# Kernel optimization log

Measured on AMD Instinct MI355X. Metric: run time of the kernel, lower is better.

The kernel has to match this reference:

```python
import jax, jax.numpy as jnp
import numpy as np
from jax import lax

C = 256          # channels
G = 16           # groups
Cg = C // G      # group channels
K = 3            # kernel size
P = K * K        # sampling points per group
PAD = 1          # spatial padding (dilation=1, stride=1)


def setup_inputs() -> dict:
    key = jax.random.key(0)
    ks = jax.random.split(key, 8)
    def rn(k, shape, s):
        return jax.random.normal(k, shape, dtype=jnp.float32) * s
    N, H, W = 4, 64, 64
    return {
        "x": jax.random.normal(ks[0], (N, C, H, W), dtype=jnp.float32),
        "w_in": rn(ks[1], (C, C), 0.02),
        "b_in": jnp.zeros((C,), jnp.float32),
        "dw_w": rn(ks[2], (C, 1, K, K), 0.1),   # depthwise conv, OIHW with I=1
        "dw_b": jnp.zeros((C,), jnp.float32),
        "ln_g": jnp.ones((C,), jnp.float32),
        "ln_b": jnp.zeros((C,), jnp.float32),
        "w_off": rn(ks[3], (C, G * P * 2), 0.01),
        "b_off": jnp.zeros((G * P * 2,), jnp.float32),
        "w_mask": rn(ks[4], (C, G * P), 0.01),
        "b_mask": jnp.zeros((G * P,), jnp.float32),
        "w_out": rn(ks[5], (C, C), 0.02),
        "b_out": jnp.zeros((C,), jnp.float32),
    }


def _layernorm(x, g, b, eps=1e-5):
    mu = jnp.mean(x, -1, keepdims=True)
    var = jnp.var(x, -1, keepdims=True)
    return (x - mu) * lax.rsqrt(var + eps) * g + b


def _dcnv3_core(xq, offset, mask, offset_scale=1.0):
    # xq: (N, Ho, Wo, C) channels-last value features (matches dcnv3_core_pytorch)
    N, Ho, Wo, _ = xq.shape
    xpad = jnp.pad(xq, ((0, 0), (PAD, PAD), (PAD, PAD), (0, 0)))
    Hi, Wi = Ho + 2 * PAD, Wo + 2 * PAD
    # reference points: pixel centers in padded coords, normalized by (Wi, Hi)
    ry = (jnp.arange(Ho, dtype=jnp.float32) + 0.5 + (K - 1) // 2) / Hi  # (Ho,)
    rx = (jnp.arange(Wo, dtype=jnp.float32) + 0.5 + (K - 1) // 2) / Wi  # (Wo,)
    # dilation grid, kw-major order as in _generate_dilation_grids
    kk = jnp.arange(K, dtype=jnp.float32) - (K - 1) // 2
    gx, gy = jnp.meshgrid(kk, kk, indexing='ij')   # gx over w, gy over h
    gpx = gx.reshape(-1) / Wi                      # (P,)
    gpy = gy.reshape(-1) / Hi
    off = offset.reshape(N, Ho, Wo, G, P, 2)
    # normalized sampling locations, shape (N, Ho, Wo, G, P)
    locx = rx[None, None, :, None, None] + gpx * offset_scale + off[..., 0] * (offset_scale / Wi)
    locy = ry[None, :, None, None, None] + gpy * offset_scale + off[..., 1] * (offset_scale / Hi)
    # grid_sample align_corners=False pixel coords
    px = locx * Wi - 0.5
    py = locy * Hi - 0.5
    x0f = jnp.floor(px); y0f = jnp.floor(py)
    fx = px - x0f; fy = py - y0f
    x0 = x0f.astype(jnp.int32); y0 = y0f.astype(jnp.int32)

    flat = jnp.transpose(xpad.reshape(N, Hi * Wi, G, Cg), (0, 2, 1, 3))  # (N,G,HiWi,Cg)

    def t(a):  # (N,Ho,Wo,G,P) -> (N,G,Ho*Wo,P)
        return jnp.transpose(a.reshape(N, Ho * Wo, G, P), (0, 2, 1, 3))

    def gather(ix, iy):
        valid = (ix >= 0) & (ix < Wi) & (iy >= 0) & (iy < Hi)
        idx = jnp.clip(iy, 0, Hi - 1) * Wi + jnp.clip(ix, 0, Wi - 1)
        idx_t = t(idx).reshape(N, G, Ho * Wo * P, 1)
        v = jnp.take_along_axis(flat, idx_t, axis=2).reshape(N, G, Ho * Wo, P, Cg)
        return v, t(valid).astype(xq.dtype)

    wx1, wy1 = t(fx), t(fy)
    wx0, wy0 = 1.0 - wx1, 1.0 - wy1
    v00, m00 = gather(x0, y0)
    v01, m01 = gather(x0 + 1, y0)
    v10, m10 = gather(x0, y0 + 1)
    v11, m11 = gather(x0 + 1, y0 + 1)
    samp = (v00 * (wx0 * wy0 * m00)[..., None] + v01 * (wx1 * wy0 * m01)[..., None]
            + v10 * (wx0 * wy1 * m10)[..., None] + v11 * (wx1 * wy1 * m11)[..., None])
    mk = t(mask)                                       # (N,G,HoWo,P)
    out = jnp.sum(samp * mk[..., None], axis=3)        # (N,G,HoWo,Cg)
    return jnp.transpose(out, (0, 2, 1, 3)).reshape(N, Ho, Wo, G * Cg)


def reference(x, w_in, b_in, dw_w, dw_b, ln_g, ln_b, w_off, b_off, w_mask, b_mask, w_out, b_out):
    N, _, H, W = x.shape
    x_nhwc = jnp.transpose(x, (0, 2, 3, 1))
    xq = x_nhwc @ w_in + b_in                          # input_proj (value branch)
    # offset/mask branch: depthwise 3x3 conv (channels_first) + LN + GELU
    x1 = lax.conv_general_dilated(x, dw_w, (1, 1), [(PAD, PAD), (PAD, PAD)],
                                  feature_group_count=C,
                                  dimension_numbers=('NCHW', 'OIHW', 'NCHW'))
    x1 = x1 + dw_b[None, :, None, None]
    x1 = jnp.transpose(x1, (0, 2, 3, 1))
    x1 = jax.nn.gelu(_layernorm(x1, ln_g, ln_b), approximate=False)
    offset = x1 @ w_off + b_off                        # (N,H,W,G*P*2)
    mask = x1 @ w_mask + b_mask                        # (N,H,W,G*P)
    mask = jax.nn.softmax(mask.reshape(N, H, W, G, P), axis=-1).reshape(N, H, W, G * P)
    y = _dcnv3_core(xq, offset, mask)
    y = y @ w_out + b_out                              # output_proj
    return jnp.transpose(y, (0, 3, 1, 2))              # back to channels_first
```

## Files before the change

### kernel.cpp

```cpp
#include <hip/hip_runtime.h>
#include <math.h>

#define CCH 256
#define HP2 68
#define WP2 68

typedef __attribute__((ext_vector_type(8))) short bf16x8;
typedef __attribute__((ext_vector_type(8))) unsigned short u16x8;
typedef __attribute__((ext_vector_type(4))) float f32x4;

__device__ __forceinline__ unsigned short f2bf(float f) {
    unsigned int u = __float_as_uint(f);
    unsigned int r = (u + 0x7fffu + ((u >> 16) & 1u)) >> 16;
    return (unsigned short)r;
}
__device__ __forceinline__ float bf2f(unsigned short h) {
    return __uint_as_float(((unsigned int)h) << 16);
}

#define OFF_XNBF   0ull
#define OFF_XPAD   8388608ull
#define OFF_X1BF   17858560ull
#define OFF_OFFS   26247168ull
#define OFF_MASK   35684352ull
#define OFF_WTIN   40402944ull
#define OFF_WTOFF  40534016ull
#define OFF_WTMSK  40681472ull
#define OFF_WTOUT  40755200ull
#define OFF_BOM    40886272ull
#define OFF_DWT    40888064ull

__global__ __launch_bounds__(256) void prep(const float* __restrict__ x,
                                            unsigned short* __restrict__ xo,
                                            unsigned int* __restrict__ xpadz,
                                            const float* __restrict__ w_in,
                                            const float* __restrict__ w_off,
                                            const float* __restrict__ w_mask,
                                            const float* __restrict__ w_out,
                                            unsigned short* __restrict__ wtin,
                                            unsigned short* __restrict__ wtoff,
                                            unsigned short* __restrict__ wtmsk,
                                            unsigned short* __restrict__ wtout,
                                            const float* __restrict__ b_off,
                                            const float* __restrict__ b_mask,
                                            float* __restrict__ bias_om,
                                            const float* __restrict__ dw_w,
                                            unsigned short* __restrict__ dwtb) {
    int z = blockIdx.z;
    int tx = threadIdx.x, ty = threadIdx.y;
    int t = ty * 32 + tx;
    if (z < 4) {
        int flat = (z * 8 + blockIdx.y) * 128 + blockIdx.x;
        for (unsigned int i = flat * 256 + t; i < 2367488u; i += 4096u * 256u) xpadz[i] = 0u;
        __shared__ float tt[32][33];
        int hw0 = blockIdx.x * 32, c0 = blockIdx.y * 32, n = z;
#pragma unroll
        for (int i = 0; i < 4; i++)
            tt[ty + i * 8][tx] = x[(size_t)(n * CCH + c0 + ty + i * 8) * 4096 + hw0 + tx];
        __syncthreads();
#pragma unroll
        for (int i = 0; i < 4; i++)
            xo[(size_t)(n * 4096 + hw0 + ty + i * 8) * CCH + c0 + tx] = f2bf(tt[tx][ty + i * 8]);
        return;
    }
    if (z == 8) {
        if (blockIdx.y == 0) {
            if (blockIdx.x < 2) {
                int i = blockIdx.x * 256 + t;
                if (i < 432) bias_om[i] = (i < 288) ? b_off[i] : b_mask[i - 288];
            } else if (blockIdx.x < 11) {
                int tap = blockIdx.x - 2;
                dwtb[tap * 256 + t] = f2bf(dw_w[t * 9 + tap]);
            }
        }
        return;
    }
    const float* w; unsigned short* wt; int N;
    if (z == 4)      { w = w_in;   wt = wtin;  N = 256; }
    else if (z == 5) { w = w_off;  wt = wtoff; N = 288; }
    else if (z == 6) { w = w_mask; wt = wtmsk; N = 144; }
    else             { w = w_out;  wt = wtout; N = 256; }
    const int K = 256;
    int n0 = blockIdx.x * 32, k0 = blockIdx.y * 32;
    if (n0 >= N) return;
    __shared__ float tb[32][33];
#pragma unroll
    for (int i = 0; i < 4; i++) {
        int k = k0 + ty + i * 8;
        if (n0 + tx < N) tb[ty + i * 8][tx] = w[(size_t)k * N + n0 + tx];
    }
    __syncthreads();
#pragma unroll
    for (int i = 0; i < 4; i++) {
        int n = n0 + ty + i * 8;
        if (n < N) wt[(size_t)n * K + k0 + tx] = f2bf(tb[tx][ty + i * 8]);
    }
}

template<int MODE>
__device__ __forceinline__ void gemm_tile(const unsigned short* __restrict__ A,
                                          const unsigned short* __restrict__ Bt,
                                          const float* __restrict__ bias,
                                          void* __restrict__ C0, void* __restrict__ C1,
                                          int N, int K, int bm, int bn, int tid) {
    int wid = tid >> 6, lane = tid & 63;
    int wr = wid >> 1, wc = wid & 1;
    int row0 = bm + wr * 64, col0 = bn + wc * 64;
    int lr = lane & 15, kg = lane >> 4;
    f32x4 acc[4][4];
#pragma unroll
    for (int i = 0; i < 4; i++)
#pragma unroll
        for (int j = 0; j < 4; j++) acc[i][j] = (f32x4){0.f, 0.f, 0.f, 0.f};

    const unsigned short* Ap = A + (size_t)(row0 + lr) * K + kg * 8;
    const unsigned short* Bp[4];
    bool bok[4];
#pragma unroll
    for (int j = 0; j < 4; j++) {
        int c = col0 + j * 16 + lr;
        bok[j] = (c < N);
        Bp[j] = Bt + (size_t)(bok[j] ? c : 0) * K + kg * 8;
    }
    const bf16x8 bzero = {0, 0, 0, 0, 0, 0, 0, 0};
    for (int k0 = 0; k0 < K; k0 += 32) {
        bf16x8 a[4], b[4];
#pragma unroll
        for (int i = 0; i < 4; i++)
            a[i] = *(const bf16x8*)(Ap + (size_t)i * 16 * K + k0);
#pragma unroll
        for (int j = 0; j < 4; j++)
            b[j] = bok[j] ? *(const bf16x8*)(Bp[j] + k0) : bzero;
        __builtin_amdgcn_s_setprio(1);
#pragma unroll
        for (int i = 0; i < 4; i++)
#pragma unroll
            for (int j = 0; j < 4; j++)
                acc[i][j] = __builtin_amdgcn_mfma_f32_16x16x32_bf16(a[i], b[j], acc[i][j], 0, 0, 0);
        __builtin_amdgcn_s_setprio(0);
    }
#pragma unroll
    for (int i = 0; i < 4; i++) {
#pragma unroll
        for (int j = 0; j < 4; j++) {
            int col = col0 + j * 16 + lr;
            if (col >= N) continue;
            float bc = (MODE == 4) ? 0.f : bias[col];
#pragma unroll
            for (int r = 0; r < 4; r++) {
                int m = row0 + i * 16 + kg * 4 + r;
                float val = acc[i][j][r] + bc;
                if (MODE == 1) {
                    int n = m >> 12, hw = m & 4095, h = hw >> 6, w = hw & 63;
                    ((unsigned short*)C0)[(size_t)((n * HP2 + h + 2) * WP2 + (w + 2)) * CCH + col] = f2bf(val);
                } else if (MODE == 4) {
                    int n = col >> 12, hw = col & 4095;
                    ((float*)C0)[(size_t)(n * CCH + m) * 4096 + hw] = val + bias[m];
                } else {
                    if (col < 288)
                        ((unsigned short*)C0)[(size_t)m * 288 + col] = f2bf(val);
                    else
                        ((unsigned short*)C1)[(size_t)m * 144 + (col - 288)] = f2bf(val);
                }
            }
        }
    }
}

template<int MODE>
__global__ __launch_bounds__(256) void gemm_mfma(const unsigned short* __restrict__ A,
                                                 const unsigned short* __restrict__ Bt,
                                                 const float* __restrict__ bias,
                                                 void* __restrict__ C0,
                                                 void* __restrict__ C1,
                                                 int N, int K) {
    gemm_tile<MODE>(A, Bt, bias, C0, C1, N, K, blockIdx.y * 128, blockIdx.x * 128, threadIdx.x);
}

__global__ __launch_bounds__(256) void stage2(const unsigned short* __restrict__ xnbf,
                                              const unsigned short* __restrict__ wtin,
                                              const float* __restrict__ b_in,
                                              unsigned short* __restrict__ xpad,
                                              const unsigned short* __restrict__ dwtb,
                                              const float* __restrict__ dw_b,
                                              const float* __restrict__ ln_g,
                                              const float* __restrict__ ln_b,
                                              unsigned short* __restrict__ x1) {
    int bid = blockIdx.x;
    if (bid < 256) {
        gemm_tile<1>(xnbf, wtin, b_in, xpad, nullptr, 256, 256,
                     (bid >> 1) * 128, (bid & 1) * 128, threadIdx.x);
        return;
    }
    int cb = bid - 256;
    int sb = (cb & 7) * 256 + (cb >> 3);
    int wid = threadIdx.x >> 6, lane = threadIdx.x & 63;
    int sub = lane >> 5, l = lane & 31;
    int m = sb * 8 + wid * 2 + sub;
    int n = m >> 12, hw = m & 4095, h = hw >> 6, w = hw & 63;
    int c0 = l << 3;
    float a[8];
    {
        float4 b0 = *(const float4*)(dw_b + c0);
        float4 b1 = *(const float4*)(dw_b + c0 + 4);
        a[0] = b0.x; a[1] = b0.y; a[2] = b0.z; a[3] = b0.w;
        a[4] = b1.x; a[5] = b1.y; a[6] = b1.z; a[7] = b1.w;
    }
#pragma unroll
    for (int ky = 0; ky < 3; ky++) {
        int hy = h + ky - 1;
        if ((unsigned)hy >= 64u) continue;
#pragma unroll
        for (int kx = 0; kx < 3; kx++) {
            int wx = w + kx - 1;
            if ((unsigned)wx >= 64u) continue;
            u16x8 xv = *(const u16x8*)(xnbf + (size_t)(n * 4096 + hy * 64 + wx) * CCH + c0);
            u16x8 wv = *(const u16x8*)(dwtb + (ky * 3 + kx) * CCH + c0);
#pragma unroll
            for (int q = 0; q < 8; q++) a[q] += bf2f(xv[q]) * bf2f(wv[q]);
        }
    }
    float s = 0.f, s2 = 0.f;
#pragma unroll
    for (int q = 0; q < 8; q++) { s += a[q]; s2 += a[q] * a[q]; }
#pragma unroll
    for (int off = 16; off; off >>= 1) {
        s += __shfl_xor(s, off);
        s2 += __shfl_xor(s2, off);
    }
    float mean = s * (1.f / 256.f);
    float var = s2 * (1.f / 256.f) - mean * mean;
    float rstd = 1.f / sqrtf(var + 1e-5f);
    float4 g0 = *(const float4*)(ln_g + c0);
    float4 g1 = *(const float4*)(ln_g + c0 + 4);
    float4 bb0 = *(const float4*)(ln_b + c0);
    float4 bb1 = *(const float4*)(ln_b + c0 + 4);
    float gg[8] = {g0.x, g0.y, g0.z, g0.w, g1.x, g1.y, g1.z, g1.w};
    float bbv[8] = {bb0.x, bb0.y, bb0.z, bb0.w, bb1.x, bb1.y, bb1.z, bb1.w};
    const float is2 = 0.70710678118654752f;
    u16x8 o;
#pragma unroll
    for (int q = 0; q < 8; q++) {
        float gv = (a[q] - mean) * rstd * gg[q] + bbv[q];
        o[q] = f2bf(0.5f * gv * (1.f + erff(gv * is2)));
    }
    *(u16x8*)(x1 + (size_t)m * CCH + c0) = o;
}

__global__ __launch_bounds__(256) void dcn_core(const unsigned short* __restrict__ xpad,
                                                const unsigned short* __restrict__ offs,
                                                const unsigned short* __restrict__ mk,
                                                unsigned short* __restrict__ y) {
    int bid = blockIdx.x;
    int sb = (bid & 7) * 256 + (bid >> 3);
    int t = sb * 256 + threadIdx.x;
    int half = t & 1, g = (t >> 1) & 15, m = t >> 5;
    int n = m >> 12, hw = m & 4095, h = hw >> 6, w = hw & 63;
    const unsigned int* op32 = (const unsigned int*)(offs + (size_t)m * 288 + g * 18);
    const unsigned short* mp = mk + ((size_t)m * 16 + g) * 9;
    const unsigned short* xb = xpad + (size_t)n * (HP2 * WP2 * CCH) + g * 16 + half * 8;

    float mv[9];
    float mx = -1e30f;
#pragma unroll
    for (int i = 0; i < 9; i++) { mv[i] = bf2f(mp[i]); mx = fmaxf(mx, mv[i]); }
    float s = 0.f;
#pragma unroll
    for (int i = 0; i < 9; i++) { mv[i] = expf(mv[i] - mx); s += mv[i]; }
    float rs = 1.f / s;

    float acc[8] = {0.f};
#pragma unroll
    for (int p = 0; p < 9; p++) {
        int dx = p / 3 - 1, dy = p % 3 - 1;
        unsigned int pk = op32[p];
        float ox = bf2f((unsigned short)(pk & 0xffffu));
        float oy = bf2f((unsigned short)(pk >> 16));
        float px = fminf(fmaxf((float)(w + 2 + dx) + ox, 0.f), 67.f);
        float py = fminf(fmaxf((float)(h + 2 + dy) + oy, 0.f), 67.f);
        float x0f = floorf(px), y0f = floorf(py);
        float fx = px - x0f, fy = py - y0f;
        int x0 = (int)x0f, y0 = (int)y0f;
        int x1c = min(x0 + 1, 67), y1c = min(y0 + 1, 67);
        float mval = mv[p] * rs;
        float w00 = (1.f - fx) * (1.f - fy) * mval;
        float w01 = fx * (1.f - fy) * mval;
        float w10 = (1.f - fx) * fy * mval;
        float w11 = fx * fy * mval;
        const unsigned short* r0 = xb + (size_t)y0 * (WP2 * CCH);
        const unsigned short* r1 = xb + (size_t)y1c * (WP2 * CCH);
        u16x8 v00 = *(const u16x8*)(r0 + x0 * CCH);
        u16x8 v01 = *(const u16x8*)(r0 + x1c * CCH);
        u16x8 v10 = *(const u16x8*)(r1 + x0 * CCH);
        u16x8 v11 = *(const u16x8*)(r1 + x1c * CCH);
#pragma unroll
        for (int q = 0; q < 8; q++)
            acc[q] += w00 * bf2f(v00[q]) + w01 * bf2f(v01[q])
                    + w10 * bf2f(v10[q]) + w11 * bf2f(v11[q]);
    }
    u16x8 v;
#pragma unroll
    for (int q = 0; q < 8; q++) v[q] = f2bf(acc[q]);
    *(u16x8*)(y + (size_t)m * CCH + g * 16 + half * 8) = v;
}

extern "C" void kernel_launch(void* const* d_in, const int* in_sizes, int n_in,
                              void* d_out, int out_size, void* d_ws, size_t ws_size,
                              hipStream_t stream) {
    const float* x      = (const float*)d_in[0];
    const float* w_in   = (const float*)d_in[1];
    const float* b_in   = (const float*)d_in[2];
    const float* dw_w   = (const float*)d_in[3];
    const float* dw_b   = (const float*)d_in[4];
    const float* ln_g   = (const float*)d_in[5];
    const float* ln_b   = (const float*)d_in[6];
    const float* w_off  = (const float*)d_in[7];
    const float* b_off  = (const float*)d_in[8];
    const float* w_mask = (const float*)d_in[9];
    const float* b_mask = (const float*)d_in[10];
    const float* w_out  = (const float*)d_in[11];
    const float* b_out  = (const float*)d_in[12];
    float* out = (float*)d_out;
    char* ws = (char*)d_ws;

    unsigned short* xnbf  = (unsigned short*)(ws + OFF_XNBF);
    unsigned short* xpad  = (unsigned short*)(ws + OFF_XPAD);
    unsigned short* x1bf  = (unsigned short*)(ws + OFF_X1BF);
    unsigned short* offs  = (unsigned short*)(ws + OFF_OFFS);
    unsigned short* mkb   = (unsigned short*)(ws + OFF_MASK);
    unsigned short* wtin  = (unsigned short*)(ws + OFF_WTIN);
    unsigned short* wtoff = (unsigned short*)(ws + OFF_WTOFF);
    unsigned short* wtmsk = (unsigned short*)(ws + OFF_WTMSK);
    unsigned short* wtout = (unsigned short*)(ws + OFF_WTOUT);
    float*          biasom = (float*)(ws + OFF_BOM);
    unsigned short* dwtb  = (unsigned short*)(ws + OFF_DWT);
    unsigned short* ybf   = xnbf;

    prep<<<dim3(128, 8, 9), dim3(32, 8), 0, stream>>>(x, xnbf, (unsigned int*)xpad,
                                                      w_in, w_off, w_mask, w_out,
                                                      wtin, wtoff, wtmsk, wtout,
                                                      b_off, b_mask, biasom, dw_w, dwtb);
    stage2<<<2304, 256, 0, stream>>>(xnbf, wtin, b_in, xpad, dwtb, dw_b, ln_g, ln_b, x1bf);
    gemm_mfma<5><<<dim3(4, 128), 256, 0, stream>>>(x1bf, wtoff, biasom, offs, mkb, 432, 256);
    dcn_core<<<2048, 256, 0, stream>>>(xpad, offs, mkb, ybf);
    gemm_mfma<4><<<dim3(128, 2), 256, 0, stream>>>(wtout, ybf, b_out, out, nullptr, 16384, 256);
}
```

Baseline: 92.69 us.

## Switch value, offset/mask and output buffers to group-major layouts

New measurement: 93.95 us. About the same (+1.4%).

```diff
diff --git a/kernel.cpp b/kernel.cpp
--- a/kernel.cpp
+++ b/kernel.cpp
@@ -4,6 +4,8 @@
 #define CCH 256
 #define HP2 68
 #define WP2 68
+#define PLANE 4624
+#define NPIX 16384
 
 typedef __attribute__((ext_vector_type(8))) short bf16x8;
 typedef __attribute__((ext_vector_type(8))) unsigned short u16x8;
@@ -21,14 +23,13 @@
 #define OFF_XNBF   0ull
 #define OFF_XPAD   8388608ull
 #define OFF_X1BF   17858560ull
-#define OFF_OFFS   26247168ull
-#define OFF_MASK   35684352ull
-#define OFF_WTIN   40402944ull
-#define OFF_WTOFF  40534016ull
-#define OFF_WTMSK  40681472ull
-#define OFF_WTOUT  40755200ull
-#define OFF_BOM    40886272ull
-#define OFF_DWT    40888064ull
+#define OFF_REC    26247168ull
+#define OFF_WTIN   43024384ull
+#define OFF_WTOFF  43155456ull
+#define OFF_WTMSK  43302912ull
+#define OFF_WTOUT  43376640ull
+#define OFF_BOM    43507712ull
+#define OFF_DWT    43509440ull
 
 __global__ __launch_bounds__(256) void prep(const float* __restrict__ x,
                                             unsigned short* __restrict__ xo,
@@ -101,7 +102,7 @@
 __device__ __forceinline__ void gemm_tile(const unsigned short* __restrict__ A,
                                           const unsigned short* __restrict__ Bt,
                                           const float* __restrict__ bias,
-                                          void* __restrict__ C0, void* __restrict__ C1,
+                                          void* __restrict__ C0,
                                           int N, int K, int bm, int bn, int tid) {
     int wid = tid >> 6, lane = tid & 63;
     int wr = wid >> 1, wc = wid & 1;
@@ -115,12 +116,17 @@
 
     const unsigned short* Ap = A + (size_t)(row0 + lr) * K + kg * 8;
     const unsigned short* Bp[4];
+    size_t cb[4];
     bool bok[4];
 #pragma unroll
     for (int j = 0; j < 4; j++) {
         int c = col0 + j * 16 + lr;
         bok[j] = (c < N);
-        Bp[j] = Bt + (size_t)(bok[j] ? c : 0) * K + kg * 8;
+        if (MODE == 4) {
+            cb[j] = (size_t)c * 16 + (kg & 1) * 8;
+        } else {
+            Bp[j] = Bt + (size_t)(bok[j] ? c : 0) * K + kg * 8;
+        }
     }
     const bf16x8 bzero = {0, 0, 0, 0, 0, 0, 0, 0};
     for (int k0 = 0; k0 < K; k0 += 32) {
@@ -129,8 +135,14 @@
         for (int i = 0; i < 4; i++)
             a[i] = *(const bf16x8*)(Ap + (size_t)i * 16 * K + k0);
 #pragma unroll
-        for (int j = 0; j < 4; j++)
-            b[j] = bok[j] ? *(const bf16x8*)(Bp[j] + k0) : bzero;
+        for (int j = 0; j < 4; j++) {
+            if (MODE == 4) {
+                size_t plane = (size_t)((k0 >> 4) + (kg >> 1)) * (16 * NPIX);
+                b[j] = *(const bf16x8*)(Bt + plane + cb[j]);
+            } else {
+                b[j] = bok[j] ? *(const bf16x8*)(Bp[j] + k0) : bzero;
+            }
+        }
         __builtin_amdgcn_s_setprio(1);
 #pragma unroll
         for (int i = 0; i < 4; i++)
@@ -152,15 +164,16 @@
                 float val = acc[i][j][r] + bc;
                 if (MODE == 1) {
                     int n = m >> 12, hw = m & 4095, h = hw >> 6, w = hw & 63;
-                    ((unsigned short*)C0)[(size_t)((n * HP2 + h + 2) * WP2 + (w + 2)) * CCH + col] = f2bf(val);
+                    int g = col >> 4, c = col & 15;
+                    ((unsigned short*)C0)[((size_t)(n * 16 + g) * PLANE + (h + 2) * WP2 + (w + 2)) * 16 + c] = f2bf(val);
                 } else if (MODE == 4) {
                     int n = col >> 12, hw = col & 4095;
                     ((float*)C0)[(size_t)(n * CCH + m) * 4096 + hw] = val + bias[m];
                 } else {
-                    if (col < 288)
-                        ((unsigned short*)C0)[(size_t)m * 288 + col] = f2bf(val);
-                    else
-                        ((unsigned short*)C1)[(size_t)m * 144 + (col - 288)] = f2bf(val);
+                    int g, j2;
+                    if (col < 288) { g = col / 18; j2 = col % 18; }
+                    else { int cc = col - 288; g = cc / 9; j2 = 18 + cc % 9; }
+                    ((unsigned short*)C0)[((size_t)g * NPIX + m) * 32 + j2] = f2bf(val);
                 }
             }
         }
@@ -172,9 +185,8 @@
                                                  const unsigned short* __restrict__ Bt,
                                                  const float* __restrict__ bias,
                                                  void* __restrict__ C0,
-                                                 void* __restrict__ C1,
                                                  int N, int K) {
-    gemm_tile<MODE>(A, Bt, bias, C0, C1, N, K, blockIdx.y * 128, blockIdx.x * 128, threadIdx.x);
+    gemm_tile<MODE>(A, Bt, bias, C0, N, K, blockIdx.y * 128, blockIdx.x * 128, threadIdx.x);
 }
 
 __global__ __launch_bounds__(256) void stage2(const unsigned short* __restrict__ xnbf,
@@ -188,7 +200,7 @@
                                               unsigned short* __restrict__ x1) {
     int bid = blockIdx.x;
     if (bid < 256) {
-        gemm_tile<1>(xnbf, wtin, b_in, xpad, nullptr, 256, 256,
+        gemm_tile<1>(xnbf, wtin, b_in, xpad, 256, 256,
                      (bid >> 1) * 128, (bid & 1) * 128, threadIdx.x);
         return;
     }
@@ -248,51 +260,63 @@
 }
 
 __global__ __launch_bounds__(256) void dcn_core(const unsigned short* __restrict__ xpad,
-                                                const unsigned short* __restrict__ offs,
-                                                const unsigned short* __restrict__ mk,
+                                                const unsigned short* __restrict__ recs,
                                                 unsigned short* __restrict__ y) {
     int bid = blockIdx.x;
     int sb = (bid & 7) * 256 + (bid >> 3);
-    int t = sb * 256 + threadIdx.x;
-    int half = t & 1, g = (t >> 1) & 15, m = t >> 5;
+    int u = sb * 256 + threadIdx.x;
+    int half = u & 1;
+    int w32 = (u >> 1) & 31;
+    int rest = u >> 6;
+    int g = rest & 15;
+    int mb = rest >> 4;
+    int m = mb * 32 + w32;
     int n = m >> 12, hw = m & 4095, h = hw >> 6, w = hw & 63;
-    const unsigned int* op32 = (const unsigned int*)(offs + (size_t)m * 288 + g * 18);
-    const unsigned short* mp = mk + ((size_t)m * 16 + g) * 9;
-    const unsigned short* xb = xpad + (size_t)n * (HP2 * WP2 * CCH) + g * 16 + half * 8;
+
+    const unsigned short* rec = recs + ((size_t)g * NPIX + m) * 32;
+    u16x8 L0 = *(const u16x8*)(rec);
+    u16x8 L1 = *(const u16x8*)(rec + 8);
+    u16x8 L2 = *(const u16x8*)(rec + 16);
+    u16x8 L3 = *(const u16x8*)(rec + 24);
+    unsigned short ctl[27];
+#pragma unroll
+    for (int e = 0; e < 8; e++) { ctl[e] = L0[e]; ctl[8 + e] = L1[e]; ctl[16 + e] = L2[e]; }
+    ctl[24] = L3[0]; ctl[25] = L3[1]; ctl[26] = L3[2];
 
     float mv[9];
     float mx = -1e30f;
 #pragma unroll
-    for (int i = 0; i < 9; i++) { mv[i] = bf2f(mp[i]); mx = fmaxf(mx, mv[i]); }
+    for (int i = 0; i < 9; i++) { mv[i] = bf2f(ctl[18 + i]); mx = fmaxf(mx, mv[i]); }
     float s = 0.f;
 #pragma unroll
     for (int i = 0; i < 9; i++) { mv[i] = expf(mv[i] - mx); s += mv[i]; }
     float rs = 1.f / s;
 
+    const unsigned short* xb = xpad + (size_t)(n * 16 + g) * (PLANE * 16) + half * 8;
+
     float acc[8] = {0.f};
 #pragma unroll
     for (int p = 0; p < 9; p++) {
         int dx = p / 3 - 1, dy = p % 3 - 1;
-        unsigned int pk = op32[p];
-        float ox = bf2f((unsigned short)(pk & 0xffffu));
-        float oy = bf2f((unsigned short)(pk >> 16));
+        float ox = bf2f(ctl[2 * p]);
+        float oy = bf2f(ctl[2 * p + 1]);
         float px = fminf(fmaxf((float)(w + 2 + dx) + ox, 0.f), 67.f);
         float py = fminf(fmaxf((float)(h + 2 + dy) + oy, 0.f), 67.f);
         float x0f = floorf(px), y0f = floorf(py);
         float fx = px - x0f, fy = py - y0f;
         int x0 = (int)x0f, y0 = (int)y0f;
-        int x1c = min(x0 + 1, 67), y1c = min(y0 + 1, 67);
+        int y1c = min(y0 + 1, 67);
         float mval = mv[p] * rs;
         float w00 = (1.f - fx) * (1.f - fy) * mval;
         float w01 = fx * (1.f - fy) * mval;
         float w10 = (1.f - fx) * fy * mval;
         float w11 = fx * fy * mval;
-        const unsigned short* r0 = xb + (size_t)y0 * (WP2 * CCH);
-        const unsigned short* r1 = xb + (size_t)y1c * (WP2 * CCH);
-        u16x8 v00 = *(const u16x8*)(r0 + x0 * CCH);
-        u16x8 v01 = *(const u16x8*)(r0 + x1c * CCH);
-        u16x8 v10 = *(const u16x8*)(r1 + x0 * CCH);
-        u16x8 v11 = *(const u16x8*)(r1 + x1c * CCH);
+        const unsigned short* r0 = xb + ((size_t)y0 * WP2 + x0) * 16;
+        const unsigned short* r1 = xb + ((size_t)y1c * WP2 + x0) * 16;
+        u16x8 v00 = *(const u16x8*)(r0);
+        u16x8 v01 = *(const u16x8*)(r0 + 16);
+        u16x8 v10 = *(const u16x8*)(r1);
+        u16x8 v11 = *(const u16x8*)(r1 + 16);
 #pragma unroll
         for (int q = 0; q < 8; q++)
             acc[q] += w00 * bf2f(v00[q]) + w01 * bf2f(v01[q])
@@ -301,7 +325,7 @@
     u16x8 v;
 #pragma unroll
     for (int q = 0; q < 8; q++) v[q] = f2bf(acc[q]);
-    *(u16x8*)(y + (size_t)m * CCH + g * 16 + half * 8) = v;
+    *(u16x8*)(y + ((size_t)g * NPIX + m) * 16 + half * 8) = v;
 }
 
 extern "C" void kernel_launch(void* const* d_in, const int* in_sizes, int n_in,
@@ -326,8 +350,7 @@
     unsigned short* xnbf  = (unsigned short*)(ws + OFF_XNBF);
     unsigned short* xpad  = (unsigned short*)(ws + OFF_XPAD);
     unsigned short* x1bf  = (unsigned short*)(ws + OFF_X1BF);
-    unsigned short* offs  = (unsigned short*)(ws + OFF_OFFS);
-    unsigned short* mkb   = (unsigned short*)(ws + OFF_MASK);
+    unsigned short* recs  = (unsigned short*)(ws + OFF_REC);
     unsigned short* wtin  = (unsigned short*)(ws + OFF_WTIN);
     unsigned short* wtoff = (unsigned short*)(ws + OFF_WTOFF);
     unsigned short* wtmsk = (unsigned short*)(ws + OFF_WTMSK);
@@ -341,7 +364,7 @@
                                                       wtin, wtoff, wtmsk, wtout,
                                                       b_off, b_mask, biasom, dw_w, dwtb);
     stage2<<<2304, 256, 0, stream>>>(xnbf, wtin, b_in, xpad, dwtb, dw_b, ln_g, ln_b, x1bf);
-    gemm_mfma<5><<<dim3(4, 128), 256, 0, stream>>>(x1bf, wtoff, biasom, offs, mkb, 432, 256);
-    dcn_core<<<2048, 256, 0, stream>>>(xpad, offs, mkb, ybf);
-    gemm_mfma<4><<<dim3(128, 2), 256, 0, stream>>>(wtout, ybf, b_out, out, nullptr, 16384, 256);
-}
+    gemm_mfma<5><<<dim3(4, 128), 256, 0, stream>>>(x1bf, wtoff, biasom, recs, 432, 256);
+    dcn_core<<<2048, 256, 0, stream>>>(xpad, recs, ybf);
+    gemm_mfma<4><<<dim3(128, 2), 256, 0, stream>>>(wtout, ybf, b_out, out, 16384, 256);
+}
```

## Stage GEMM tiles through LDS with global_load_lds instead of direct register loads

Applied to the files above, without the earlier changes.

New measurement: 80.44 us. 13.2% less time.

```diff
diff --git a/kernel.cpp b/kernel.cpp
--- a/kernel.cpp
+++ b/kernel.cpp
@@ -4,6 +4,7 @@
 #define CCH 256
 #define HP2 68
 #define WP2 68
+#define NPIX 16384
 
 typedef __attribute__((ext_vector_type(8))) short bf16x8;
 typedef __attribute__((ext_vector_type(8))) unsigned short u16x8;
@@ -16,6 +17,13 @@
 }
 __device__ __forceinline__ float bf2f(unsigned short h) {
     return __uint_as_float(((unsigned int)h) << 16);
+}
+
+__device__ __forceinline__ void gll16(const unsigned short* g, unsigned short* l) {
+    __builtin_amdgcn_global_load_lds(
+        (const __attribute__((address_space(1))) unsigned int*)g,
+        (__attribute__((address_space(3))) unsigned int*)l,
+        16, 0, 0);
 }
 
 #define OFF_XNBF   0ull
@@ -26,9 +34,10 @@
 #define OFF_WTIN   40402944ull
 #define OFF_WTOFF  40534016ull
 #define OFF_WTMSK  40681472ull
-#define OFF_WTOUT  40755200ull
-#define OFF_BOM    40886272ull
-#define OFF_DWT    40888064ull
+#define OFF_BPAD   40755200ull
+#define OFF_WTOUT  40796160ull
+#define OFF_BOM    40927232ull
+#define OFF_DWT    40928960ull
 
 __global__ __launch_bounds__(256) void prep(const float* __restrict__ x,
                                             unsigned short* __restrict__ xo,
@@ -45,7 +54,8 @@
                                             const float* __restrict__ b_mask,
                                             float* __restrict__ bias_om,
                                             const float* __restrict__ dw_w,
-                                            unsigned short* __restrict__ dwtb) {
+                                            unsigned short* __restrict__ dwtb,
+                                            unsigned int* __restrict__ bpad) {
     int z = blockIdx.z;
     int tx = threadIdx.x, ty = threadIdx.y;
     int t = ty * 32 + tx;
@@ -71,6 +81,8 @@
             } else if (blockIdx.x < 11) {
                 int tap = blockIdx.x - 2;
                 dwtb[tap * 256 + t] = f2bf(dw_w[t * 9 + tap]);
+            } else if (blockIdx.x < 51) {
+                bpad[(blockIdx.x - 11) * 256 + t] = 0u;
             }
         }
         return;
@@ -102,35 +114,42 @@
                                           const unsigned short* __restrict__ Bt,
                                           const float* __restrict__ bias,
                                           void* __restrict__ C0, void* __restrict__ C1,
-                                          int N, int K, int bm, int bn, int tid) {
+                                          int N, int K, int bm, int bn, int tid,
+                                          unsigned short* As, unsigned short* Bs) {
     int wid = tid >> 6, lane = tid & 63;
     int wr = wid >> 1, wc = wid & 1;
-    int row0 = bm + wr * 64, col0 = bn + wc * 64;
     int lr = lane & 15, kg = lane >> 4;
+    int r = lane >> 2, q = lane & 3;
+
+    const unsigned short* Ag0 = A + (size_t)(bm + 32 * wid + r) * K + q * 8;
+    const unsigned short* Ag1 = Ag0 + (size_t)16 * K;
+    const unsigned short* Bg0 = Bt + (size_t)(bn + 32 * wid + r) * K + q * 8;
+    const unsigned short* Bg1 = Bg0 + (size_t)16 * K;
+    unsigned short* Al0 = As + wid * 1024;
+    unsigned short* Al1 = Al0 + 512;
+    unsigned short* Bl0 = Bs + wid * 1024;
+    unsigned short* Bl1 = Bl0 + 512;
+
+    const unsigned short* Ar = As + (wr * 64 + lr) * 32 + kg * 8;
+    const unsigned short* Br = Bs + (wc * 64 + lr) * 32 + kg * 8;
+
     f32x4 acc[4][4];
 #pragma unroll
     for (int i = 0; i < 4; i++)
 #pragma unroll
         for (int j = 0; j < 4; j++) acc[i][j] = (f32x4){0.f, 0.f, 0.f, 0.f};
 
-    const unsigned short* Ap = A + (size_t)(row0 + lr) * K + kg * 8;
-    const unsigned short* Bp[4];
-    bool bok[4];
-#pragma unroll
-    for (int j = 0; j < 4; j++) {
-        int c = col0 + j * 16 + lr;
-        bok[j] = (c < N);
-        Bp[j] = Bt + (size_t)(bok[j] ? c : 0) * K + kg * 8;
-    }
-    const bf16x8 bzero = {0, 0, 0, 0, 0, 0, 0, 0};
     for (int k0 = 0; k0 < K; k0 += 32) {
+        gll16(Ag0 + k0, Al0);
+        gll16(Ag1 + k0, Al1);
+        gll16(Bg0 + k0, Bl0);
+        gll16(Bg1 + k0, Bl1);
+        __syncthreads();
         bf16x8 a[4], b[4];
 #pragma unroll
-        for (int i = 0; i < 4; i++)
-            a[i] = *(const bf16x8*)(Ap + (size_t)i * 16 * K + k0);
-#pragma unroll
-        for (int j = 0; j < 4; j++)
-            b[j] = bok[j] ? *(const bf16x8*)(Bp[j] + k0) : bzero;
+        for (int i = 0; i < 4; i++) a[i] = *(const bf16x8*)(Ar + i * 512);
+#pragma unroll
+        for (int j = 0; j < 4; j++) b[j] = *(const bf16x8*)(Br + j * 512);
         __builtin_amdgcn_s_setprio(1);
 #pragma unroll
         for (int i = 0; i < 4; i++)
@@ -138,7 +157,10 @@
             for (int j = 0; j < 4; j++)
                 acc[i][j] = __builtin_amdgcn_mfma_f32_16x16x32_bf16(a[i], b[j], acc[i][j], 0, 0, 0);
         __builtin_amdgcn_s_setprio(0);
-    }
+        __syncthreads();
+    }
+
+    int row0 = bm + wr * 64, col0 = bn + wc * 64;
 #pragma unroll
     for (int i = 0; i < 4; i++) {
 #pragma unroll
@@ -147,9 +169,9 @@
             if (col >= N) continue;
             float bc = (MODE == 4) ? 0.f : bias[col];
 #pragma unroll
-            for (int r = 0; r < 4; r++) {
-                int m = row0 + i * 16 + kg * 4 + r;
-                float val = acc[i][j][r] + bc;
+            for (int r2 = 0; r2 < 4; r2++) {
+                int m = row0 + i * 16 + kg * 4 + r2;
+                float val = acc[i][j][r2] + bc;
                 if (MODE == 1) {
                     int n = m >> 12, hw = m & 4095, h = hw >> 6, w = hw & 63;
                     ((unsigned short*)C0)[(size_t)((n * HP2 + h + 2) * WP2 + (w + 2)) * CCH + col] = f2bf(val);
@@ -174,7 +196,10 @@
                                                  void* __restrict__ C0,
                                                  void* __restrict__ C1,
                                                  int N, int K) {
-    gemm_tile<MODE>(A, Bt, bias, C0, C1, N, K, blockIdx.y * 128, blockIdx.x * 128, threadIdx.x);
+    __shared__ unsigned short As[4096];
+    __shared__ unsigned short Bs[4096];
+    gemm_tile<MODE>(A, Bt, bias, C0, C1, N, K, blockIdx.y * 128, blockIdx.x * 128,
+                    threadIdx.x, As, Bs);
 }
 
 __global__ __launch_bounds__(256) void stage2(const unsigned short* __restrict__ xnbf,
@@ -186,10 +211,12 @@
                                               const float* __restrict__ ln_g,
                                               const float* __restrict__ ln_b,
                                               unsigned short* __restrict__ x1) {
+    __shared__ unsigned short As[4096];
+    __shared__ unsigned short Bs[4096];
     int bid = blockIdx.x;
     if (bid < 256) {
         gemm_tile<1>(xnbf, wtin, b_in, xpad, nullptr, 256, 256,
-                     (bid >> 1) * 128, (bid & 1) * 128, threadIdx.x);
+                     (bid >> 1) * 128, (bid & 1) * 128, threadIdx.x, As, Bs);
         return;
     }
     int cb = bid - 256;
@@ -331,6 +358,7 @@
     unsigned short* wtin  = (unsigned short*)(ws + OFF_WTIN);
     unsigned short* wtoff = (unsigned short*)(ws + OFF_WTOFF);
     unsigned short* wtmsk = (unsigned short*)(ws + OFF_WTMSK);
+    unsigned int*   bpad  = (unsigned int*)(ws + OFF_BPAD);
     unsigned short* wtout = (unsigned short*)(ws + OFF_WTOUT);
     float*          biasom = (float*)(ws + OFF_BOM);
     unsigned short* dwtb  = (unsigned short*)(ws + OFF_DWT);
@@ -339,7 +367,7 @@
     prep<<<dim3(128, 8, 9), dim3(32, 8), 0, stream>>>(x, xnbf, (unsigned int*)xpad,
                                                       w_in, w_off, w_mask, w_out,
                                                       wtin, wtoff, wtmsk, wtout,
-                                                      b_off, b_mask, biasom, dw_w, dwtb);
+                                                      b_off, b_mask, biasom, dw_w, dwtb, bpad);
     stage2<<<2304, 256, 0, stream>>>(xnbf, wtin, b_in, xpad, dwtb, dw_b, ln_g, ln_b, x1bf);
     gemm_mfma<5><<<dim3(4, 128), 256, 0, stream>>>(x1bf, wtoff, biasom, offs, mkb, 432, 256);
     dcn_core<<<2048, 256, 0, stream>>>(xpad, offs, mkb, ybf);
```
